# Kernel optimization log

Measured on AMD Instinct MI355X. Metric: run time of the kernel, lower is better.

The kernel has to match this reference:

```python
import jax, jax.numpy as jnp
import numpy as np

N = 50000   # nodes
E = 800000  # edges (before self loops)
F = 128     # in_dim
H = 4       # heads
C = 32      # hidden_dim per head
HC = H * C  # 128 == F
L = 3       # n_layers
G = 64      # graphs in batch
OUT = 64    # out_dim
NEG_SLOPE = 0.2


def setup_inputs() -> dict:
    key = jax.random.key(0)
    ks = jax.random.split(key, 12)
    s = 0.1
    x = jax.random.normal(ks[0], (N, F), jnp.float32)
    src = jax.random.randint(ks[1], (E,), 0, N, dtype=jnp.int32)
    dst = jax.random.randint(ks[2], (E,), 0, N, dtype=jnp.int32)
    # even split into G graphs so no graph is empty (segment_max safe)
    batch = (jnp.arange(N, dtype=jnp.int32) * G // N).astype(jnp.int32)
    Ws = jax.random.normal(ks[3], (L, HC, HC), jnp.float32) * s       # layer0 in=F=HC
    att_src = jax.random.normal(ks[4], (L, H, C), jnp.float32) * s
    att_dst = jax.random.normal(ks[5], (L, H, C), jnp.float32) * s
    conv_b = jnp.zeros((L, HC), jnp.float32)
    gate_W = jax.random.normal(ks[6], (L + 1, HC, 1), jnp.float32) * s
    gate_b = jnp.zeros((L + 1,), jnp.float32)
    lin_W = jax.random.normal(ks[7], (L + 1, HC, OUT), jnp.float32) * s
    lin_b = jnp.zeros((L + 1, OUT), jnp.float32)
    h_weights = jnp.ones((L + 1,), jnp.float32) / (L + 1)
    h0 = jax.random.normal(ks[8], (1,), jnp.float32)
    beta = jax.random.normal(ks[9], (OUT,), jnp.float32) * s
    pool_w = jnp.ones((3,), jnp.float32) / 3.0
    return dict(x=x, src=src, dst=dst, batch=batch, Ws=Ws, att_src=att_src,
                att_dst=att_dst, conv_b=conv_b, gate_W=gate_W, gate_b=gate_b,
                lin_W=lin_W, lin_b=lin_b, h_weights=h_weights, h0=h0,
                beta=beta, pool_w=pool_w)


def _seg_softmax(e, idx, n):
    # numerically stable softmax within segments
    m = jax.ops.segment_max(e, idx, num_segments=n)
    m = jnp.where(jnp.isfinite(m), m, 0.0)
    ex = jnp.exp(e - m[idx])
    s = jax.ops.segment_sum(ex, idx, num_segments=n)
    return ex / (s[idx] + 1e-16)


def _gat_layer(x, src, dst, W, a_src, a_dst, b):
    h = (x @ W).reshape(N, H, C)               # [N,H,C]
    al_s = jnp.sum(h * a_src, axis=-1)         # [N,H]
    al_d = jnp.sum(h * a_dst, axis=-1)         # [N,H]
    e = jax.nn.leaky_relu(al_s[src] + al_d[dst], NEG_SLOPE)  # [E+N,H]
    alpha = _seg_softmax(e, dst, N)            # softmax over incoming edges
    msg = h[src] * alpha[..., None]            # [E+N,H,C]
    out = jax.ops.segment_sum(msg, dst, num_segments=N)
    return out.reshape(N, HC) + b


def _pool_block(x, gw, gb, pool_w, batch, counts):
    gate = jax.nn.sigmoid(x @ gw + gb)[:, 0]          # [N]
    a = _seg_softmax(gate, batch, G)                  # per-graph attention
    p_att = jax.ops.segment_sum(a[:, None] * x, batch, num_segments=G)
    p_mean = jax.ops.segment_sum(x, batch, num_segments=G) / counts[:, None]
    p_max = jax.ops.segment_max(x, batch, num_segments=G)
    return pool_w[0] * p_att + pool_w[1] * p_mean + pool_w[2] * p_max


def reference(x, src, dst, batch, Ws, att_src, att_dst, conv_b, gate_W,
              gate_b, lin_W, lin_b, h_weights, h0, beta, pool_w):
    loops = jnp.arange(N, dtype=src.dtype)
    src_sl = jnp.concatenate([src, loops])
    dst_sl = jnp.concatenate([dst, loops])
    counts = jax.ops.segment_sum(jnp.ones((N,), x.dtype), batch, num_segments=G)
    out = jnp.zeros((G, OUT), x.dtype)
    for i in range(L):
        p = _pool_block(x, gate_W[i], gate_b[i], pool_w, batch, counts)
        out = out + h_weights[i] * (p @ lin_W[i] + lin_b[i])
        x = _gat_layer(x, src_sl, dst_sl, Ws[i], att_src[i], att_dst[i], conv_b[i])
        if i != L - 1:
            x = jax.nn.relu(x)
    p = _pool_block(x, gate_W[L], gate_b[L], pool_w, batch, counts)
    out = out + h_weights[L] * (p @ lin_W[L] + lin_b[L])
    risk_score = out @ beta + h0[0]   # [G]
    return risk_score
```

## Files before the change

kernel.cpp:

```cpp
#include <hip/hip_runtime.h>
#include <hip/hip_fp16.h>
#include <math.h>

#define N_NODES 50000
#define N_EDGES 800000
#define HC 128
#define NH 4
#define NG 64
#define NOUT 64
#define NLAYERS 3
#define POOL_CHUNKS 16
#define CAST_BLOCKS (N_NODES * HC / 4 / 256)
#define PREPW_BLOCKS (NLAYERS * HC * HC / 256)
#define NBKT ((N_NODES + 127) / 128)
#define PB_BLOCKS ((N_EDGES + 4095) / 4096)
#define GEMM_BLOCKS ((N_NODES + 15) / 16)
#define POOL2_BLOCKS (NG * POOL_CHUNKS / 2)
#define XT_STRIDE 136
#define ZREG_FLOATS ((NLAYERS + 1) * NG * HC * 2 + (NLAYERS + 1) * NG)
#define ZREG_BLOCKS ((ZREG_FLOATS / 4 + 255) / 256)
#define PMAX_BLOCKS ((NLAYERS + 1) * NG * HC / 4 / 256)
#define LOG2E 1.44269504f

typedef _Float16 v4h __attribute__((ext_vector_type(4)));
typedef float v4f __attribute__((ext_vector_type(4)));

__device__ __forceinline__ void graph_range(int g, int* start, int* end) {
    *start = (int)(((long long)g * N_NODES + NG - 1) / NG);
    *end   = (int)(((long long)(g + 1) * N_NODES + NG - 1) / NG);
}

__device__ __forceinline__ float atomicMaxFloat(float* addr, float val) {
    if (val >= 0.f)
        return __int_as_float(atomicMax((int*)addr, __float_as_int(val)));
    else
        return __uint_as_float(atomicMin((unsigned int*)addr, __float_as_uint(val)));
}


__device__ __forceinline__ void gemm_body(
        int b, const __half* __restrict__ x, const _Float16* __restrict__ Wt,
        const float* __restrict__ a_src, const float* __restrict__ a_dst,
        __half* __restrict__ hh, float* __restrict__ al_s, float* __restrict__ al_d) {
    __shared__ __align__(16) _Float16 xt[16][XT_STRIDE];
    int t = threadIdx.x;
    int w = t >> 6;
    int l = t & 63;
    int n0 = b * 16;
    {
        uint4 v = ((const uint4*)(x + (size_t)n0 * HC))[t];
        *(uint4*)&xt[t >> 4][(t & 15) * 8] = v;
    }
    __syncthreads();
    int m = l & 15;
    int kg = (l >> 4) * 4;
    v4h a[8];
#pragma unroll
    for (int ks = 0; ks < 8; ks++)
        a[ks] = *(const v4h*)&xt[m][kg + ks * 16];
    __syncthreads();
    const _Float16* bp0 = Wt + (uint)(w * 32 + m) * HC + kg;
    const _Float16* bp1 = bp0 + 16 * HC;
    v4f acc0 = {0.f, 0.f, 0.f, 0.f}, acc1 = {0.f, 0.f, 0.f, 0.f};
#pragma unroll
    for (int ks = 0; ks < 8; ks++) {
        v4h b0 = *(const v4h*)(bp0 + ks * 16);
        v4h b1 = *(const v4h*)(bp1 + ks * 16);
        acc0 = __builtin_amdgcn_mfma_f32_16x16x16f16(a[ks], b0, acc0, 0, 0, 0);
        acc1 = __builtin_amdgcn_mfma_f32_16x16x16f16(a[ks], b1, acc1, 0, 0, 0);
    }
    int d0 = w * 32 + m;
    float as0 = a_src[d0] * LOG2E,      ad0 = a_dst[d0] * LOG2E;
    float as1 = a_src[d0 + 16] * LOG2E, ad1 = a_dst[d0 + 16] * LOG2E;
    int rloc = (l >> 4) * 4;
#pragma unroll
    for (int r = 0; r < 4; r++) {
        int n = n0 + rloc + r;
        xt[rloc + r][d0]      = (_Float16)acc0[r];
        xt[rloc + r][d0 + 16] = (_Float16)acc1[r];
        float vs = acc0[r] * as0 + acc1[r] * as1;
        float vd = acc0[r] * ad0 + acc1[r] * ad1;
#pragma unroll
        for (int mk = 8; mk >= 1; mk >>= 1) {
            vs += __shfl_xor(vs, mk);
            vd += __shfl_xor(vd, mk);
        }
        if ((l & 15) == 0) {
            al_s[(uint)(n * NH + w)] = vs;
            al_d[(uint)(n * NH + w)] = vd;
        }
    }
    __syncthreads();
    uint4 v = *(const uint4*)&xt[t >> 4][(t & 15) * 8];
    ((uint4*)(hh + (size_t)n0 * HC))[t] = v;
}

__device__ __forceinline__ void pool_body(
        int b, const __half* __restrict__ x, const float* __restrict__ gate,
        float* __restrict__ p_att, float* __restrict__ p_sum,
        float* __restrict__ p_max, float* __restrict__ wsum) {
    int c = b * 2 + (threadIdx.x >> 7);
    int g = c >> 4;
    int chunk = c & 15;
    int d = threadIdx.x & 127;
    int start, end; graph_range(g, &start, &end);
    int cnt = end - start;
    int cstart = start + (cnt * chunk) / POOL_CHUNKS;
    int cend   = start + (cnt * (chunk + 1)) / POOL_CHUNKS;
    float aat = 0.f, asu = 0.f, amx = -INFINITY, ws = 0.f;
    int n = cstart;
    for (; n + 4 <= cend; n += 4) {
        float w0 = gate[n],     w1 = gate[n + 1];
        float w2 = gate[n + 2], w3 = gate[n + 3];
        float x0 = __half2float(x[(uint)((n + 0) * HC + d)]);
        float x1 = __half2float(x[(uint)((n + 1) * HC + d)]);
        float x2 = __half2float(x[(uint)((n + 2) * HC + d)]);
        float x3 = __half2float(x[(uint)((n + 3) * HC + d)]);
        aat = fmaf(w0, x0, aat); aat = fmaf(w1, x1, aat);
        aat = fmaf(w2, x2, aat); aat = fmaf(w3, x3, aat);
        asu += (x0 + x1) + (x2 + x3);
        amx = fmaxf(amx, fmaxf(fmaxf(x0, x1), fmaxf(x2, x3)));
        ws += (w0 + w1) + (w2 + w3);
    }
    for (; n < cend; n++) {
        float w = gate[n];
        float xv = __half2float(x[(uint)(n * HC + d)]);
        aat = fmaf(w, xv, aat);
        asu += xv;
        amx = fmaxf(amx, xv);
        ws += w;
    }
    atomicAdd(&p_att[g * HC + d], aat);
    atomicAdd(&p_sum[g * HC + d], asu);
    atomicMaxFloat(&p_max[g * HC + d], amx);
    if (d == 0) atomicAdd(&wsum[g], ws);
}

__device__ __forceinline__ void scat2_body(
        int bkt, const int2* __restrict__ part, const int* __restrict__ bktbase,
        int* __restrict__ rowptr, int* __restrict__ csr_src) {
    __shared__ int degs[128];
    __shared__ int curs[128];
    __shared__ int w0tot;
    int t = threadIdx.x;
    int nstart = bkt << 7;
    int nend = nstart + 128; if (nend > N_NODES) nend = N_NODES;
    int nloc = nend - nstart;
    int estart = bktbase[bkt], eend = bktbase[bkt + 1];
    if (t < 128) degs[t] = 0;
    __syncthreads();
    for (int e = estart + t; e < eend; e += 256)
        atomicAdd(&degs[part[e].y - nstart], 1);
    __syncthreads();
    int v = 0, inc = 0;
    if (t < 128) {
        v = degs[t];
        inc = v;
#pragma unroll
        for (int off = 1; off < 64; off <<= 1) {
            int u = __shfl_up(inc, off);
            if ((t & 63) >= off) inc += u;
        }
    }
    if (t == 63) w0tot = inc;
    __syncthreads();
    if (t < 128) {
        int excl = inc - v + ((t >= 64) ? w0tot : 0);
        int rp = estart + excl;
        curs[t] = rp;
        if (t < nloc) rowptr[nstart + t] = rp;
    }
    __syncthreads();
    for (int e = estart + t; e < eend; e += 256) {
        int2 p = part[e];
        int pos = atomicAdd(&curs[p.y - nstart], 1);
        csr_src[pos] = p.x;
    }
}


__global__ __launch_bounds__(256) void k_prep(
        const float* __restrict__ x, __half* __restrict__ xh,
        const float* __restrict__ Ws, _Float16* __restrict__ Wt,
        const int* __restrict__ dst, int* __restrict__ bh,
        const float* __restrict__ gw, const float* __restrict__ gbp,
        float* __restrict__ gate,
        float* __restrict__ zreg, uint* __restrict__ pmaxw) {
    int b = blockIdx.x;
    int t = threadIdx.x;
    if (b < CAST_BLOCKS) {
        uint i = b * 256 + t;
        float4 v = ((const float4*)x)[i];
        __half2 a = __floats2half2_rn(v.x, v.y);
        __half2 c = __floats2half2_rn(v.z, v.w);
        ((__half2*)xh)[2 * i] = a;
        ((__half2*)xh)[2 * i + 1] = c;
        float4 gwv = ((const float4*)gw)[t & 31];
        float dot = v.x * gwv.x + v.y * gwv.y + v.z * gwv.z + v.w * gwv.w;
#pragma unroll
        for (int m = 16; m >= 1; m >>= 1) dot += __shfl_xor(dot, m);
        if ((t & 31) == 0) {
            int n = b * 8 + (t >> 5);
            float sg = 1.f / (1.f + __expf(-(dot + gbp[0])));
            gate[n] = __expf(sg);
        }
    } else if (b < CAST_BLOCKS + PREPW_BLOCKS) {
        int e = (b - CAST_BLOCKS) * 256 + t;
        int layer = e >> 14; int r = e & 16383; int k = r >> 7; int d = r & 127;
        Wt[layer * 16384 + d * 128 + k] = (_Float16)Ws[layer * 16384 + k * 128 + d];
    } else if (b < CAST_BLOCKS + PREPW_BLOCKS + PB_BLOCKS) {
        int pb = b - CAST_BLOCKS - PREPW_BLOCKS;
        __shared__ int cnt[NBKT];
        for (int i = t; i < NBKT; i += 256) cnt[i] = 0;
        __syncthreads();
        int base = pb * 4096;
#pragma unroll
        for (int k = 0; k < 16; k++) {
            int e = base + t + 256 * k;
            if (e < N_EDGES) atomicAdd(&cnt[dst[e] >> 7], 1);
        }
        __syncthreads();
        for (int i = t; i < NBKT; i += 256) bh[i * PB_BLOCKS + pb] = cnt[i];
    } else {
        int zb = b - CAST_BLOCKS - PREPW_BLOCKS - PB_BLOCKS;
        if (zb < ZREG_BLOCKS) {
            int i = zb * 256 + t;
            if (i < ZREG_FLOATS / 4)
                ((float4*)zreg)[i] = make_float4(0.f, 0.f, 0.f, 0.f);
        } else {
            int i = (zb - ZREG_BLOCKS) * 256 + t;
            uint4 f; f.x = f.y = f.z = f.w = 0xFFFFFFFFu;
            ((uint4*)pmaxw)[i] = f;
        }
    }
}

__global__ __launch_bounds__(256) void k_scan_bh(int* __restrict__ bh,
                                                 int* __restrict__ bkttot) {
    __shared__ int tmp[256];
    int bkt = blockIdx.x, t = threadIdx.x;
    int v = (t < PB_BLOCKS) ? bh[bkt * PB_BLOCKS + t] : 0;
    tmp[t] = v;
    __syncthreads();
    for (int off = 1; off < 256; off <<= 1) {
        int u = (t >= off) ? tmp[t - off] : 0;
        __syncthreads();
        tmp[t] += u;
        __syncthreads();
    }
    if (t < PB_BLOCKS) bh[bkt * PB_BLOCKS + t] = tmp[t] - v;
    if (t == 255) bkttot[bkt] = tmp[255];
}

__global__ __launch_bounds__(512) void k_bktbase(const int* __restrict__ bkttot,
                                                 int* __restrict__ bktbase,
                                                 int* __restrict__ rowptr) {
    __shared__ int tmp[512];
    int t = threadIdx.x;
    int v = (t < NBKT) ? bkttot[t] : 0;
    tmp[t] = v;
    __syncthreads();
    for (int off = 1; off < 512; off <<= 1) {
        int u = (t >= off) ? tmp[t - off] : 0;
        __syncthreads();
        tmp[t] += u;
        __syncthreads();
    }
    if (t < NBKT) bktbase[t] = tmp[t] - v;
    if (t == NBKT - 1) {
        bktbase[NBKT] = tmp[t];
        rowptr[N_NODES] = tmp[t];
    }
}

__global__ __launch_bounds__(256) void k_part(
        const int* __restrict__ src, const int* __restrict__ dst,
        const int* __restrict__ bktbase, const int* __restrict__ bh,
        int2* __restrict__ part) {
    __shared__ int curs[NBKT];
    int blk = blockIdx.x, t = threadIdx.x;
    for (int i = t; i < NBKT; i += 256)
        curs[i] = bktbase[i] + bh[i * PB_BLOCKS + blk];
    __syncthreads();
    int base = blk * 4096;
#pragma unroll
    for (int k = 0; k < 16; k++) {
        int e = base + t + 256 * k;
        if (e < N_EDGES) {
            int d = dst[e];
            int pos = atomicAdd(&curs[d >> 7], 1);
            part[pos] = make_int2(src[e], d);
        }
    }
}


__global__ __launch_bounds__(256) void k_fused_a2(
        const int2* __restrict__ part, const int* __restrict__ bktbase,
        int* __restrict__ rowptr, int* __restrict__ csr_src,
        const __half* __restrict__ x0h, const _Float16* __restrict__ Wt,
        const float* __restrict__ a_src, const float* __restrict__ a_dst,
        __half* __restrict__ hh, float* __restrict__ al_s, float* __restrict__ al_d,
        const float* __restrict__ gate,
        float* __restrict__ p_att, float* __restrict__ p_sum,
        float* __restrict__ p_max, float* __restrict__ wsum) {
    int b = blockIdx.x;
    if (b < NBKT) {
        scat2_body(b, part, bktbase, rowptr, csr_src);
    } else if (b < NBKT + GEMM_BLOCKS) {
        gemm_body(b - NBKT, x0h, Wt, a_src, a_dst, hh, al_s, al_d);
    } else {
        pool_body(b - NBKT - GEMM_BLOCKS, x0h, gate, p_att, p_sum, p_max, wsum);
    }
}

__global__ __launch_bounds__(256) void k_fused_b(
        const __half* __restrict__ x, const _Float16* __restrict__ Wt,
        const float* __restrict__ a_src, const float* __restrict__ a_dst,
        __half* __restrict__ hh, float* __restrict__ al_s, float* __restrict__ al_d,
        const float* __restrict__ gate,
        float* __restrict__ p_att, float* __restrict__ p_sum,
        float* __restrict__ p_max, float* __restrict__ wsum) {
    int b = blockIdx.x;
    if (b < GEMM_BLOCKS) {
        gemm_body(b, x, Wt, a_src, a_dst, hh, al_s, al_d);
    } else {
        pool_body(b - GEMM_BLOCKS, x, gate, p_att, p_sum, p_max, wsum);
    }
}

__global__ __launch_bounds__(256) void k_pool(
        const __half* __restrict__ x, const float* __restrict__ gate,
        float* __restrict__ p_att, float* __restrict__ p_sum,
        float* __restrict__ p_max, float* __restrict__ wsum) {
    pool_body(blockIdx.x, x, gate, p_att, p_sum, p_max, wsum);
}


__global__ __launch_bounds__(256) void k_agg(
        const __half* __restrict__ hh, const float* __restrict__ al_s,
        const float* __restrict__ al_d, const int* __restrict__ rowptr,
        const int* __restrict__ csr_src, const float* __restrict__ conv_b,
        __half* __restrict__ xout, int do_relu,
        const float* __restrict__ gw, const float* __restrict__ gbp,
        float* __restrict__ gate) {
    int n = (blockIdx.x * blockDim.x + threadIdx.x) >> 6;
    if (n >= N_NODES) return;
    int l = threadIdx.x & 63;
    int head = l >> 4;
    int le = l & 15;
    int grp4 = (l & 48) << 2;
    float ad = al_d[(uint)(n * NH + head)];
    const __half2* hh2 = (const __half2*)hh;
    float e0 = al_s[(uint)(n * NH + head)] + ad;
    e0 = fmaxf(e0, 0.2f * e0);
    float s_uni = exp2f(e0);
    float2 vself = __half22float2(hh2[(uint)(n * 64 + l)]);
    float ax = s_uni * vself.x, ay = s_uni * vself.y;
    int jb = rowptr[n], je = rowptr[n + 1];
    float s_part = 0.f;
    for (int j = jb; j < je; j += 16) {
        int rem = je - j;
        bool act = le < rem;
        int my_s = csr_src[j + (act ? le : 0)];
        float aa = al_s[(uint)(my_s * NH + head)];
        float e = aa + ad;
        e = fmaxf(e, 0.2f * e);
        float ex = act ? exp2f(e) : 0.f;
        s_part += ex;
        int exb = __float_as_int(ex);
        __half2 vv[16];
#pragma unroll
        for (int u = 0; u < 16; u++) {
            int ssu = __builtin_amdgcn_readlane(my_s, u);
            const __half2* rp = hh2 + ((size_t)(uint)ssu << 6);
            vv[u] = rp[l];
        }
#pragma unroll
        for (int u = 0; u < 16; u++) {
            float exu = __int_as_float(
                __builtin_amdgcn_ds_bpermute(grp4 + 4 * u, exb));
            float2 vf = __half22float2(vv[u]);
            ax = fmaf(exu, vf.x, ax);
            ay = fmaf(exu, vf.y, ay);
        }
    }
    s_part += __shfl_xor(s_part, 1);
    s_part += __shfl_xor(s_part, 2);
    s_part += __shfl_xor(s_part, 4);
    s_part += __shfl_xor(s_part, 8);
    float s = s_part + s_uni;
    float inv = 1.f / (s + 1e-16f);
    float2 cb = ((const float2*)conv_b)[l];
    float r0 = fmaf(ax, inv, cb.x);
    float r1 = fmaf(ay, inv, cb.y);
    if (do_relu) { r0 = fmaxf(r0, 0.f); r1 = fmaxf(r1, 0.f); }
    ((__half2*)xout)[(uint)(n * 64 + l)] = __floats2half2_rn(r0, r1);
    float2 gwv = ((const float2*)gw)[l];
    float gv = r0 * gwv.x + r1 * gwv.y;
#pragma unroll
    for (int m = 32; m >= 1; m >>= 1) gv += __shfl_xor(gv, m);
    if (l == 0) {
        float sg = 1.f / (1.f + __expf(-(gv + gbp[0])));
        gate[n] = __expf(sg);
    }
}


__global__ __launch_bounds__(128) void k_finish(
        const float* __restrict__ p_att, const float* __restrict__ p_sum,
        const float* __restrict__ p_max, const float* __restrict__ wsum,
        const float* __restrict__ pool_w, const float* __restrict__ lin_W,
        const float* __restrict__ lin_b, const float* __restrict__ hw,
        const float* __restrict__ beta, const float* __restrict__ h0,
        float* __restrict__ out) {
    int g = blockIdx.x, t = threadIdx.x;
    __shared__ float p[NLAYERS + 1][HC];
    int start, end; graph_range(g, &start, &end);
    float cinv = 1.f / (float)(end - start);
    float pw0 = pool_w[0], pw1 = pool_w[1], pw2 = pool_w[2];
#pragma unroll
    for (int j = 0; j <= NLAYERS; j++) {
        float winv = 1.f / (wsum[j * NG + g] + 1e-16f);
        p[j][t] = pw0 * p_att[(j * NG + g) * HC + t] * winv
                + pw1 * p_sum[(j * NG + g) * HC + t] * cinv
                + pw2 * p_max[(j * NG + g) * HC + t];
    }
    __syncthreads();
    if (t < NOUT) {
        float acc = 0.f;
#pragma unroll
        for (int j = 0; j <= NLAYERS; j++) {
            float a = lin_b[j * NOUT + t];
            const float* Wj = lin_W + (size_t)j * HC * NOUT;
            for (int k = 0; k < HC; k++) a = fmaf(p[j][k], Wj[k * NOUT + t], a);
            acc = fmaf(hw[j], a, acc);
        }
        float v = acc * beta[t];
#pragma unroll
        for (int m = 32; m >= 1; m >>= 1) v += __shfl_xor(v, m);
        if (t == 0) out[g] = v + h0[0];
    }
}


extern "C" void kernel_launch(void* const* d_in, const int* in_sizes, int n_in,
                              void* d_out, int out_size, void* d_ws, size_t ws_size,
                              hipStream_t stream) {
    const float* x0       = (const float*)d_in[0];
    const int*   src      = (const int*)d_in[1];
    const int*   dst      = (const int*)d_in[2];
    const float* Ws       = (const float*)d_in[4];
    const float* att_src  = (const float*)d_in[5];
    const float* att_dst  = (const float*)d_in[6];
    const float* conv_b   = (const float*)d_in[7];
    const float* gate_W   = (const float*)d_in[8];
    const float* gate_b   = (const float*)d_in[9];
    const float* lin_W    = (const float*)d_in[10];
    const float* lin_b    = (const float*)d_in[11];
    const float* h_w      = (const float*)d_in[12];
    const float* h0       = (const float*)d_in[13];
    const float* beta     = (const float*)d_in[14];
    const float* pool_w   = (const float*)d_in[15];

    char* base = (char*)d_ws;
    size_t off = 0;
    auto carve = [&](size_t bytes) -> char* {
        char* p = base + off;
        off = (off + bytes + 255) & ~(size_t)255;
        return p;
    };
    __half*    x0h     = (__half*)carve((size_t)N_NODES * HC * 2);
    __half*    xA      = (__half*)carve((size_t)N_NODES * HC * 2);
    __half*    xB      = (__half*)carve((size_t)N_NODES * HC * 2);
    __half*    hh      = (__half*)carve((size_t)N_NODES * HC * 2);
    _Float16*  Wt      = (_Float16*)carve((size_t)NLAYERS * HC * HC * 2);
    float*     al_s    = (float*)carve((size_t)N_NODES * NH * 4);
    float*     al_d    = (float*)carve((size_t)N_NODES * NH * 4);
    float*     gate    = (float*)carve((size_t)N_NODES * 4);
    int*       rowptr  = (int*)carve((size_t)(N_NODES + 1) * 4);
    int*       csrsrc  = (int*)carve((size_t)N_EDGES * 4);
    int*       bh      = (int*)carve((size_t)NBKT * PB_BLOCKS * 4);
    int*       bkttot  = (int*)carve((size_t)NBKT * 4);
    int*       bktbase = (int*)carve((size_t)(NBKT + 1) * 4);
    int2*      part    = (int2*)carve((size_t)N_EDGES * 8);
    float*     zreg    = (float*)carve((size_t)ZREG_FLOATS * 4);
    float*     p_att   = zreg;
    float*     p_sum   = zreg + (size_t)(NLAYERS + 1) * NG * HC;
    float*     wsum    = p_sum + (size_t)(NLAYERS + 1) * NG * HC;
    float*     p_max   = (float*)carve((size_t)(NLAYERS + 1) * NG * HC * 4);

    k_prep<<<CAST_BLOCKS + PREPW_BLOCKS + PB_BLOCKS + ZREG_BLOCKS + PMAX_BLOCKS,
             256, 0, stream>>>(
        x0, x0h, Ws, Wt, dst, bh, gate_W, gate_b, gate, zreg, (uint*)p_max);

    k_scan_bh<<<NBKT, 256, 0, stream>>>(bh, bkttot);
    k_bktbase<<<1, 512, 0, stream>>>(bkttot, bktbase, rowptr);
    k_part<<<PB_BLOCKS, 256, 0, stream>>>(src, dst, bktbase, bh, part);

    k_fused_a2<<<NBKT + GEMM_BLOCKS + POOL2_BLOCKS, 256, 0, stream>>>(
        part, bktbase, rowptr, csrsrc,
        x0h, Wt, att_src, att_dst, hh, al_s, al_d,
        gate, p_att, p_sum, p_max, wsum);

    __half* xbufs[3] = { xA, xB, xA };
    for (int i = 0; i < NLAYERS; i++) {
        __half* xnext = xbufs[i];
        int j = i + 1;
        k_agg<<<(N_NODES + 3) / 4, 256, 0, stream>>>(hh, al_s, al_d, rowptr, csrsrc,
                                                     conv_b + i * HC, xnext,
                                                     (i != NLAYERS - 1) ? 1 : 0,
                                                     gate_W + j * HC, gate_b + j,
                                                     gate);
        if (i + 1 < NLAYERS) {
            k_fused_b<<<GEMM_BLOCKS + POOL2_BLOCKS, 256, 0, stream>>>(
                xnext, Wt + (size_t)(i + 1) * HC * HC,
                att_src + (i + 1) * HC, att_dst + (i + 1) * HC,
                hh, al_s, al_d,
                gate,
                p_att + (size_t)j * NG * HC,
                p_sum + (size_t)j * NG * HC,
                p_max + (size_t)j * NG * HC,
                wsum + j * NG);
        } else {
            k_pool<<<POOL2_BLOCKS, 256, 0, stream>>>(
                xnext, gate,
                p_att + (size_t)j * NG * HC,
                p_sum + (size_t)j * NG * HC,
                p_max + (size_t)j * NG * HC,
                wsum + j * NG);
        }
    }

    k_finish<<<NG, 128, 0, stream>>>(p_att, p_sum, p_max, wsum, pool_w,
                                     lin_W, lin_b, h_w, beta, h0, (float*)d_out);
}
```

Baseline: 270.9 us.

## Fuse input cast and gate into first GEMM, pack edge partitions, reschedule pooling

The fp32→fp16 cast of x and the gate computation move out of the prep kernel and into the first GEMM, which reads fp32 x directly and writes x0h. Edge partition entries are packed into one int (16-bit src, 7-bit local dst), which halves partition traffic but relies on N fitting in 16 bits. Layer-0 pooling now runs in the same launch as the first aggregation, with double-buffered gate arrays, so more independent work shares each launch. The bpermute broadcast in aggregation is replaced by ds_swizzle.

Result: faster. 264.5 us (-2.4%).

```diff
diff --git a/kernel.cpp b/kernel.cpp
--- a/kernel.cpp
+++ b/kernel.cpp
@@ -10,12 +10,12 @@
 #define NOUT 64
 #define NLAYERS 3
 #define POOL_CHUNKS 16
-#define CAST_BLOCKS (N_NODES * HC / 4 / 256)
 #define PREPW_BLOCKS (NLAYERS * HC * HC / 256)
 #define NBKT ((N_NODES + 127) / 128)
 #define PB_BLOCKS ((N_EDGES + 4095) / 4096)
 #define GEMM_BLOCKS ((N_NODES + 15) / 16)
 #define POOL2_BLOCKS (NG * POOL_CHUNKS / 2)
+#define AGG_BLOCKS ((N_NODES + 3) / 4)
 #define XT_STRIDE 136
 #define ZREG_FLOATS ((NLAYERS + 1) * NG * HC * 2 + (NLAYERS + 1) * NG)
 #define ZREG_BLOCKS ((ZREG_FLOATS / 4 + 255) / 256)
@@ -38,17 +38,51 @@
 }
 
 
+template<bool F32>
 __device__ __forceinline__ void gemm_body(
-        int b, const __half* __restrict__ x, const _Float16* __restrict__ Wt,
+        int b, const void* xin, const _Float16* __restrict__ Wt,
         const float* __restrict__ a_src, const float* __restrict__ a_dst,
-        __half* __restrict__ hh, float* __restrict__ al_s, float* __restrict__ al_d) {
+        __half* __restrict__ hh, float* __restrict__ al_s, float* __restrict__ al_d,
+        __half* __restrict__ xh_out, const float* __restrict__ gw,
+        const float* __restrict__ gbp, float* __restrict__ gate) {
     __shared__ __align__(16) _Float16 xt[16][XT_STRIDE];
     int t = threadIdx.x;
     int w = t >> 6;
     int l = t & 63;
     int n0 = b * 16;
-    {
-        uint4 v = ((const uint4*)(x + (size_t)n0 * HC))[t];
+    if constexpr (F32) {
+        const float4* xg = (const float4*)((const float*)xin + (size_t)n0 * HC);
+        float4 v0 = xg[t];
+        float4 v1 = xg[t + 256];
+        float4 gwv = ((const float4*)gw)[t & 31];
+        float p0 = v0.x * gwv.x + v0.y * gwv.y + v0.z * gwv.z + v0.w * gwv.w;
+        float p1 = v1.x * gwv.x + v1.y * gwv.y + v1.z * gwv.z + v1.w * gwv.w;
+#pragma unroll
+        for (int mk = 16; mk >= 1; mk >>= 1) {
+            p0 += __shfl_xor(p0, mk);
+            p1 += __shfl_xor(p1, mk);
+        }
+        if ((t & 31) == 0) {
+            int r = t >> 5;
+            float sg0 = 1.f / (1.f + __expf(-(p0 + gbp[0])));
+            float sg1 = 1.f / (1.f + __expf(-(p1 + gbp[0])));
+            gate[n0 + r]     = __expf(sg0);
+            gate[n0 + 8 + r] = __expf(sg1);
+        }
+        __half2 h00 = __floats2half2_rn(v0.x, v0.y);
+        __half2 h01 = __floats2half2_rn(v0.z, v0.w);
+        __half2 h10 = __floats2half2_rn(v1.x, v1.y);
+        __half2 h11 = __floats2half2_rn(v1.z, v1.w);
+        uint2 pa, pb;
+        pa.x = *(const uint*)&h00; pa.y = *(const uint*)&h01;
+        pb.x = *(const uint*)&h10; pb.y = *(const uint*)&h11;
+        int row = t >> 5, colh = (t & 31) * 4;
+        *(uint2*)&xt[row][colh] = pa;
+        *(uint2*)&xt[row + 8][colh] = pb;
+        ((uint2*)xh_out)[(size_t)n0 * (HC / 4) + t]       = pa;
+        ((uint2*)xh_out)[(size_t)n0 * (HC / 4) + t + 256] = pb;
+    } else {
+        uint4 v = ((const uint4*)((const __half*)xin + (size_t)n0 * HC))[t];
         *(uint4*)&xt[t >> 4][(t & 15) * 8] = v;
     }
     __syncthreads();
@@ -137,7 +171,7 @@
 }
 
 __device__ __forceinline__ void scat2_body(
-        int bkt, const int2* __restrict__ part, const int* __restrict__ bktbase,
+        int bkt, const int* __restrict__ part, const int* __restrict__ bktbase,
         int* __restrict__ rowptr, int* __restrict__ csr_src) {
     __shared__ int degs[128];
     __shared__ int curs[128];
@@ -150,7 +184,7 @@
     if (t < 128) degs[t] = 0;
     __syncthreads();
     for (int e = estart + t; e < eend; e += 256)
-        atomicAdd(&degs[part[e].y - nstart], 1);
+        atomicAdd(&degs[(part[e] >> 16) & 127], 1);
     __syncthreads();
     int v = 0, inc = 0;
     if (t < 128) {
@@ -172,184 +206,24 @@
     }
     __syncthreads();
     for (int e = estart + t; e < eend; e += 256) {
-        int2 p = part[e];
-        int pos = atomicAdd(&curs[p.y - nstart], 1);
-        csr_src[pos] = p.x;
-    }
-}
-
-
-__global__ __launch_bounds__(256) void k_prep(
-        const float* __restrict__ x, __half* __restrict__ xh,
-        const float* __restrict__ Ws, _Float16* __restrict__ Wt,
-        const int* __restrict__ dst, int* __restrict__ bh,
-        const float* __restrict__ gw, const float* __restrict__ gbp,
-        float* __restrict__ gate,
-        float* __restrict__ zreg, uint* __restrict__ pmaxw) {
-    int b = blockIdx.x;
-    int t = threadIdx.x;
-    if (b < CAST_BLOCKS) {
-        uint i = b * 256 + t;
-        float4 v = ((const float4*)x)[i];
-        __half2 a = __floats2half2_rn(v.x, v.y);
-        __half2 c = __floats2half2_rn(v.z, v.w);
-        ((__half2*)xh)[2 * i] = a;
-        ((__half2*)xh)[2 * i + 1] = c;
-        float4 gwv = ((const float4*)gw)[t & 31];
-        float dot = v.x * gwv.x + v.y * gwv.y + v.z * gwv.z + v.w * gwv.w;
-#pragma unroll
-        for (int m = 16; m >= 1; m >>= 1) dot += __shfl_xor(dot, m);
-        if ((t & 31) == 0) {
-            int n = b * 8 + (t >> 5);
-            float sg = 1.f / (1.f + __expf(-(dot + gbp[0])));
-            gate[n] = __expf(sg);
-        }
-    } else if (b < CAST_BLOCKS + PREPW_BLOCKS) {
-        int e = (b - CAST_BLOCKS) * 256 + t;
-        int layer = e >> 14; int r = e & 16383; int k = r >> 7; int d = r & 127;
-        Wt[layer * 16384 + d * 128 + k] = (_Float16)Ws[layer * 16384 + k * 128 + d];
-    } else if (b < CAST_BLOCKS + PREPW_BLOCKS + PB_BLOCKS) {
-        int pb = b - CAST_BLOCKS - PREPW_BLOCKS;
-        __shared__ int cnt[NBKT];
-        for (int i = t; i < NBKT; i += 256) cnt[i] = 0;
-        __syncthreads();
-        int base = pb * 4096;
-#pragma unroll
-        for (int k = 0; k < 16; k++) {
-            int e = base + t + 256 * k;
-            if (e < N_EDGES) atomicAdd(&cnt[dst[e] >> 7], 1);
-        }
-        __syncthreads();
-        for (int i = t; i < NBKT; i += 256) bh[i * PB_BLOCKS + pb] = cnt[i];
-    } else {
-        int zb = b - CAST_BLOCKS - PREPW_BLOCKS - PB_BLOCKS;
-        if (zb < ZREG_BLOCKS) {
-            int i = zb * 256 + t;
-            if (i < ZREG_FLOATS / 4)
-                ((float4*)zreg)[i] = make_float4(0.f, 0.f, 0.f, 0.f);
-        } else {
-            int i = (zb - ZREG_BLOCKS) * 256 + t;
-            uint4 f; f.x = f.y = f.z = f.w = 0xFFFFFFFFu;
-            ((uint4*)pmaxw)[i] = f;
-        }
-    }
-}
-
-__global__ __launch_bounds__(256) void k_scan_bh(int* __restrict__ bh,
-                                                 int* __restrict__ bkttot) {
-    __shared__ int tmp[256];
-    int bkt = blockIdx.x, t = threadIdx.x;
-    int v = (t < PB_BLOCKS) ? bh[bkt * PB_BLOCKS + t] : 0;
-    tmp[t] = v;
-    __syncthreads();
-    for (int off = 1; off < 256; off <<= 1) {
-        int u = (t >= off) ? tmp[t - off] : 0;
-        __syncthreads();
-        tmp[t] += u;
-        __syncthreads();
-    }
-    if (t < PB_BLOCKS) bh[bkt * PB_BLOCKS + t] = tmp[t] - v;
-    if (t == 255) bkttot[bkt] = tmp[255];
-}
-
-__global__ __launch_bounds__(512) void k_bktbase(const int* __restrict__ bkttot,
-                                                 int* __restrict__ bktbase,
-                                                 int* __restrict__ rowptr) {
-    __shared__ int tmp[512];
-    int t = threadIdx.x;
-    int v = (t < NBKT) ? bkttot[t] : 0;
-    tmp[t] = v;
-    __syncthreads();
-    for (int off = 1; off < 512; off <<= 1) {
-        int u = (t >= off) ? tmp[t - off] : 0;
-        __syncthreads();
-        tmp[t] += u;
-        __syncthreads();
-    }
-    if (t < NBKT) bktbase[t] = tmp[t] - v;
-    if (t == NBKT - 1) {
-        bktbase[NBKT] = tmp[t];
-        rowptr[N_NODES] = tmp[t];
-    }
-}
-
-__global__ __launch_bounds__(256) void k_part(
-        const int* __restrict__ src, const int* __restrict__ dst,
-        const int* __restrict__ bktbase, const int* __restrict__ bh,
-        int2* __restrict__ part) {
-    __shared__ int curs[NBKT];
-    int blk = blockIdx.x, t = threadIdx.x;
-    for (int i = t; i < NBKT; i += 256)
-        curs[i] = bktbase[i] + bh[i * PB_BLOCKS + blk];
-    __syncthreads();
-    int base = blk * 4096;
-#pragma unroll
-    for (int k = 0; k < 16; k++) {
-        int e = base + t + 256 * k;
-        if (e < N_EDGES) {
-            int d = dst[e];
-            int pos = atomicAdd(&curs[d >> 7], 1);
-            part[pos] = make_int2(src[e], d);
-        }
-    }
-}
-
-
-__global__ __launch_bounds__(256) void k_fused_a2(
-        const int2* __restrict__ part, const int* __restrict__ bktbase,
-        int* __restrict__ rowptr, int* __restrict__ csr_src,
-        const __half* __restrict__ x0h, const _Float16* __restrict__ Wt,
-        const float* __restrict__ a_src, const float* __restrict__ a_dst,
-        __half* __restrict__ hh, float* __restrict__ al_s, float* __restrict__ al_d,
-        const float* __restrict__ gate,
-        float* __restrict__ p_att, float* __restrict__ p_sum,
-        float* __restrict__ p_max, float* __restrict__ wsum) {
-    int b = blockIdx.x;
-    if (b < NBKT) {
-        scat2_body(b, part, bktbase, rowptr, csr_src);
-    } else if (b < NBKT + GEMM_BLOCKS) {
-        gemm_body(b - NBKT, x0h, Wt, a_src, a_dst, hh, al_s, al_d);
-    } else {
-        pool_body(b - NBKT - GEMM_BLOCKS, x0h, gate, p_att, p_sum, p_max, wsum);
-    }
-}
-
-__global__ __launch_bounds__(256) void k_fused_b(
-        const __half* __restrict__ x, const _Float16* __restrict__ Wt,
-        const float* __restrict__ a_src, const float* __restrict__ a_dst,
-        __half* __restrict__ hh, float* __restrict__ al_s, float* __restrict__ al_d,
-        const float* __restrict__ gate,
-        float* __restrict__ p_att, float* __restrict__ p_sum,
-        float* __restrict__ p_max, float* __restrict__ wsum) {
-    int b = blockIdx.x;
-    if (b < GEMM_BLOCKS) {
-        gemm_body(b, x, Wt, a_src, a_dst, hh, al_s, al_d);
-    } else {
-        pool_body(b - GEMM_BLOCKS, x, gate, p_att, p_sum, p_max, wsum);
-    }
-}
-
-__global__ __launch_bounds__(256) void k_pool(
-        const __half* __restrict__ x, const float* __restrict__ gate,
-        float* __restrict__ p_att, float* __restrict__ p_sum,
-        float* __restrict__ p_max, float* __restrict__ wsum) {
-    pool_body(blockIdx.x, x, gate, p_att, p_sum, p_max, wsum);
-}
-
-
-__global__ __launch_bounds__(256) void k_agg(
-        const __half* __restrict__ hh, const float* __restrict__ al_s,
+        int p = part[e];
+        int pos = atomicAdd(&curs[(p >> 16) & 127], 1);
+        csr_src[pos] = p & 0xFFFF;
+    }
+}
+
+__device__ __forceinline__ void agg_body(
+        int b, const __half* __restrict__ hh, const float* __restrict__ al_s,
         const float* __restrict__ al_d, const int* __restrict__ rowptr,
         const int* __restrict__ csr_src, const float* __restrict__ conv_b,
         __half* __restrict__ xout, int do_relu,
         const float* __restrict__ gw, const float* __restrict__ gbp,
         float* __restrict__ gate) {
-    int n = (blockIdx.x * blockDim.x + threadIdx.x) >> 6;
+    int n = b * 4 + (threadIdx.x >> 6);
     if (n >= N_NODES) return;
     int l = threadIdx.x & 63;
     int head = l >> 4;
     int le = l & 15;
-    int grp4 = (l & 48) << 2;
     float ad = al_d[(uint)(n * NH + head)];
     const __half2* hh2 = (const __half2*)hh;
     float e0 = al_s[(uint)(n * NH + head)] + ad;
@@ -376,14 +250,18 @@
             const __half2* rp = hh2 + ((size_t)(uint)ssu << 6);
             vv[u] = rp[l];
         }
-#pragma unroll
-        for (int u = 0; u < 16; u++) {
-            float exu = __int_as_float(
-                __builtin_amdgcn_ds_bpermute(grp4 + 4 * u, exb));
-            float2 vf = __half22float2(vv[u]);
-            ax = fmaf(exu, vf.x, ax);
-            ay = fmaf(exu, vf.y, ay);
-        }
+#define AGG_SLOT(U) {                                                        \
+            float exu = __int_as_float(                                      \
+                __builtin_amdgcn_ds_swizzle(exb, 16 + 32 * (U)));            \
+            float2 vf = __half22float2(vv[U]);                               \
+            ax = fmaf(exu, vf.x, ax);                                        \
+            ay = fmaf(exu, vf.y, ay);                                        \
+        }
+        AGG_SLOT(0)  AGG_SLOT(1)  AGG_SLOT(2)  AGG_SLOT(3)
+        AGG_SLOT(4)  AGG_SLOT(5)  AGG_SLOT(6)  AGG_SLOT(7)
+        AGG_SLOT(8)  AGG_SLOT(9)  AGG_SLOT(10) AGG_SLOT(11)
+        AGG_SLOT(12) AGG_SLOT(13) AGG_SLOT(14) AGG_SLOT(15)
+#undef AGG_SLOT
     }
     s_part += __shfl_xor(s_part, 1);
     s_part += __shfl_xor(s_part, 2);
@@ -404,6 +282,174 @@
         float sg = 1.f / (1.f + __expf(-(gv + gbp[0])));
         gate[n] = __expf(sg);
     }
+}
+
+
+__global__ __launch_bounds__(256) void k_prep(
+        const float* __restrict__ Ws, _Float16* __restrict__ Wt,
+        const int* __restrict__ dst, int* __restrict__ bh,
+        float* __restrict__ zreg, uint* __restrict__ pmaxw) {
+    int b = blockIdx.x;
+    int t = threadIdx.x;
+    if (b < PREPW_BLOCKS) {
+        int e = b * 256 + t;
+        int layer = e >> 14; int r = e & 16383; int k = r >> 7; int d = r & 127;
+        Wt[layer * 16384 + d * 128 + k] = (_Float16)Ws[layer * 16384 + k * 128 + d];
+    } else if (b < PREPW_BLOCKS + PB_BLOCKS) {
+        int pb = b - PREPW_BLOCKS;
+        __shared__ int cnt[NBKT];
+        for (int i = t; i < NBKT; i += 256) cnt[i] = 0;
+        __syncthreads();
+        int base = pb * 4096;
+#pragma unroll
+        for (int k = 0; k < 16; k++) {
+            int e = base + t + 256 * k;
+            if (e < N_EDGES) atomicAdd(&cnt[dst[e] >> 7], 1);
+        }
+        __syncthreads();
+        for (int i = t; i < NBKT; i += 256) bh[i * PB_BLOCKS + pb] = cnt[i];
+    } else {
+        int zb = b - PREPW_BLOCKS - PB_BLOCKS;
+        if (zb < ZREG_BLOCKS) {
+            int i = zb * 256 + t;
+            if (i < ZREG_FLOATS / 4)
+                ((float4*)zreg)[i] = make_float4(0.f, 0.f, 0.f, 0.f);
+        } else {
+            int i = (zb - ZREG_BLOCKS) * 256 + t;
+            uint4 f; f.x = f.y = f.z = f.w = 0xFFFFFFFFu;
+            ((uint4*)pmaxw)[i] = f;
+        }
+    }
+}
+
+__global__ __launch_bounds__(256) void k_scan_bh(int* __restrict__ bh,
+                                                 int* __restrict__ bkttot) {
+    __shared__ int tmp[256];
+    int bkt = blockIdx.x, t = threadIdx.x;
+    int v = (t < PB_BLOCKS) ? bh[bkt * PB_BLOCKS + t] : 0;
+    tmp[t] = v;
+    __syncthreads();
+    for (int off = 1; off < 256; off <<= 1) {
+        int u = (t >= off) ? tmp[t - off] : 0;
+        __syncthreads();
+        tmp[t] += u;
+        __syncthreads();
+    }
+    if (t < PB_BLOCKS) bh[bkt * PB_BLOCKS + t] = tmp[t] - v;
+    if (t == 255) bkttot[bkt] = tmp[255];
+}
+
+__global__ __launch_bounds__(512) void k_bktbase(const int* __restrict__ bkttot,
+                                                 int* __restrict__ bktbase,
+                                                 int* __restrict__ rowptr) {
+    __shared__ int tmp[512];
+    int t = threadIdx.x;
+    int v = (t < NBKT) ? bkttot[t] : 0;
+    tmp[t] = v;
+    __syncthreads();
+    for (int off = 1; off < 512; off <<= 1) {
+        int u = (t >= off) ? tmp[t - off] : 0;
+        __syncthreads();
+        tmp[t] += u;
+        __syncthreads();
+    }
+    if (t < NBKT) bktbase[t] = tmp[t] - v;
+    if (t == NBKT - 1) {
+        bktbase[NBKT] = tmp[t];
+        rowptr[N_NODES] = tmp[t];
+    }
+}
+
+__global__ __launch_bounds__(256) void k_part(
+        const int* __restrict__ src, const int* __restrict__ dst,
+        const int* __restrict__ bktbase, const int* __restrict__ bh,
+        int* __restrict__ part) {
+    __shared__ int curs[NBKT];
+    int blk = blockIdx.x, t = threadIdx.x;
+    for (int i = t; i < NBKT; i += 256)
+        curs[i] = bktbase[i] + bh[i * PB_BLOCKS + blk];
+    __syncthreads();
+    int base = blk * 4096;
+#pragma unroll
+    for (int k = 0; k < 16; k++) {
+        int e = base + t + 256 * k;
+        if (e < N_EDGES) {
+            int d = dst[e];
+            int pos = atomicAdd(&curs[d >> 7], 1);
+            part[pos] = src[e] | ((d & 127) << 16);
+        }
+    }
+}
+
+
+__global__ __launch_bounds__(256) void k_fused_a2(
+        const int* __restrict__ part, const int* __restrict__ bktbase,
+        int* __restrict__ rowptr, int* __restrict__ csr_src,
+        const float* __restrict__ x0, const _Float16* __restrict__ Wt,
+        const float* __restrict__ a_src, const float* __restrict__ a_dst,
+        __half* __restrict__ hh, float* __restrict__ al_s, float* __restrict__ al_d,
+        __half* __restrict__ x0h, const float* __restrict__ gw,
+        const float* __restrict__ gbp, float* __restrict__ gate) {
+    int b = blockIdx.x;
+    if (b < NBKT) {
+        scat2_body(b, part, bktbase, rowptr, csr_src);
+    } else {
+        gemm_body<true>(b - NBKT, x0, Wt, a_src, a_dst, hh, al_s, al_d,
+                        x0h, gw, gbp, gate);
+    }
+}
+
+__global__ __launch_bounds__(256) void k_fused_agg(
+        const __half* __restrict__ hh, const float* __restrict__ al_s,
+        const float* __restrict__ al_d, const int* __restrict__ rowptr,
+        const int* __restrict__ csr_src, const float* __restrict__ conv_b,
+        __half* __restrict__ xout, int do_relu,
+        const float* __restrict__ gw, const float* __restrict__ gbp,
+        float* __restrict__ gate_out,
+        const __half* __restrict__ xp, const float* __restrict__ gate_in,
+        float* __restrict__ p_att, float* __restrict__ p_sum,
+        float* __restrict__ p_max, float* __restrict__ wsum) {
+    int b = blockIdx.x;
+    if (b < POOL2_BLOCKS) {
+        pool_body(b, xp, gate_in, p_att, p_sum, p_max, wsum);
+    } else {
+        agg_body(b - POOL2_BLOCKS, hh, al_s, al_d, rowptr, csr_src, conv_b,
+                 xout, do_relu, gw, gbp, gate_out);
+    }
+}
+
+__global__ __launch_bounds__(256) void k_fused_b(
+        const __half* __restrict__ x, const _Float16* __restrict__ Wt,
+        const float* __restrict__ a_src, const float* __restrict__ a_dst,
+        __half* __restrict__ hh, float* __restrict__ al_s, float* __restrict__ al_d,
+        const float* __restrict__ gate,
+        float* __restrict__ p_att, float* __restrict__ p_sum,
+        float* __restrict__ p_max, float* __restrict__ wsum) {
+    int b = blockIdx.x;
+    if (b < GEMM_BLOCKS) {
+        gemm_body<false>(b, x, Wt, a_src, a_dst, hh, al_s, al_d,
+                         nullptr, nullptr, nullptr, nullptr);
+    } else {
+        pool_body(b - GEMM_BLOCKS, x, gate, p_att, p_sum, p_max, wsum);
+    }
+}
+
+__global__ __launch_bounds__(256) void k_agg(
+        const __half* __restrict__ hh, const float* __restrict__ al_s,
+        const float* __restrict__ al_d, const int* __restrict__ rowptr,
+        const int* __restrict__ csr_src, const float* __restrict__ conv_b,
+        __half* __restrict__ xout, int do_relu,
+        const float* __restrict__ gw, const float* __restrict__ gbp,
+        float* __restrict__ gate) {
+    agg_body(blockIdx.x, hh, al_s, al_d, rowptr, csr_src, conv_b,
+             xout, do_relu, gw, gbp, gate);
+}
+
+__global__ __launch_bounds__(256) void k_pool(
+        const __half* __restrict__ x, const float* __restrict__ gate,
+        float* __restrict__ p_att, float* __restrict__ p_sum,
+        float* __restrict__ p_max, float* __restrict__ wsum) {
+    pool_body(blockIdx.x, x, gate, p_att, p_sum, p_max, wsum);
 }
 
 
@@ -477,60 +523,61 @@
     _Float16*  Wt      = (_Float16*)carve((size_t)NLAYERS * HC * HC * 2);
     float*     al_s    = (float*)carve((size_t)N_NODES * NH * 4);
     float*     al_d    = (float*)carve((size_t)N_NODES * NH * 4);
-    float*     gate    = (float*)carve((size_t)N_NODES * 4);
+    float*     gateA   = (float*)carve((size_t)N_NODES * 4);
+    float*     gateB   = (float*)carve((size_t)N_NODES * 4);
     int*       rowptr  = (int*)carve((size_t)(N_NODES + 1) * 4);
     int*       csrsrc  = (int*)carve((size_t)N_EDGES * 4);
     int*       bh      = (int*)carve((size_t)NBKT * PB_BLOCKS * 4);
     int*       bkttot  = (int*)carve((size_t)NBKT * 4);
     int*       bktbase = (int*)carve((size_t)(NBKT + 1) * 4);
-    int2*      part    = (int2*)carve((size_t)N_EDGES * 8);
+    int*       part    = (int*)carve((size_t)N_EDGES * 4);
     float*     zreg    = (float*)carve((size_t)ZREG_FLOATS * 4);
     float*     p_att   = zreg;
     float*     p_sum   = zreg + (size_t)(NLAYERS + 1) * NG * HC;
     float*     wsum    = p_sum + (size_t)(NLAYERS + 1) * NG * HC;
     float*     p_max   = (float*)carve((size_t)(NLAYERS + 1) * NG * HC * 4);
 
-    k_prep<<<CAST_BLOCKS + PREPW_BLOCKS + PB_BLOCKS + ZREG_BLOCKS + PMAX_BLOCKS,
-             256, 0, stream>>>(
-        x0, x0h, Ws, Wt, dst, bh, gate_W, gate_b, gate, zreg, (uint*)p_max);
+    k_prep<<<PREPW_BLOCKS + PB_BLOCKS + ZREG_BLOCKS + PMAX_BLOCKS, 256, 0, stream>>>(
+        Ws, Wt, dst, bh, zreg, (uint*)p_max);
 
     k_scan_bh<<<NBKT, 256, 0, stream>>>(bh, bkttot);
     k_bktbase<<<1, 512, 0, stream>>>(bkttot, bktbase, rowptr);
     k_part<<<PB_BLOCKS, 256, 0, stream>>>(src, dst, bktbase, bh, part);
 
-    k_fused_a2<<<NBKT + GEMM_BLOCKS + POOL2_BLOCKS, 256, 0, stream>>>(
+    k_fused_a2<<<NBKT + GEMM_BLOCKS, 256, 0, stream>>>(
         part, bktbase, rowptr, csrsrc,
-        x0h, Wt, att_src, att_dst, hh, al_s, al_d,
-        gate, p_att, p_sum, p_max, wsum);
-
-    __half* xbufs[3] = { xA, xB, xA };
-    for (int i = 0; i < NLAYERS; i++) {
-        __half* xnext = xbufs[i];
-        int j = i + 1;
-        k_agg<<<(N_NODES + 3) / 4, 256, 0, stream>>>(hh, al_s, al_d, rowptr, csrsrc,
-                                                     conv_b + i * HC, xnext,
-                                                     (i != NLAYERS - 1) ? 1 : 0,
-                                                     gate_W + j * HC, gate_b + j,
-                                                     gate);
-        if (i + 1 < NLAYERS) {
-            k_fused_b<<<GEMM_BLOCKS + POOL2_BLOCKS, 256, 0, stream>>>(
-                xnext, Wt + (size_t)(i + 1) * HC * HC,
-                att_src + (i + 1) * HC, att_dst + (i + 1) * HC,
-                hh, al_s, al_d,
-                gate,
-                p_att + (size_t)j * NG * HC,
-                p_sum + (size_t)j * NG * HC,
-                p_max + (size_t)j * NG * HC,
-                wsum + j * NG);
-        } else {
-            k_pool<<<POOL2_BLOCKS, 256, 0, stream>>>(
-                xnext, gate,
-                p_att + (size_t)j * NG * HC,
-                p_sum + (size_t)j * NG * HC,
-                p_max + (size_t)j * NG * HC,
-                wsum + j * NG);
-        }
-    }
+        x0, Wt, att_src, att_dst, hh, al_s, al_d,
+        x0h, gate_W, gate_b, gateA);
+
+    k_fused_agg<<<POOL2_BLOCKS + AGG_BLOCKS, 256, 0, stream>>>(
+        hh, al_s, al_d, rowptr, csrsrc, conv_b,
+        xA, 1, gate_W + HC, gate_b + 1, gateB,
+        x0h, gateA, p_att, p_sum, p_max, wsum);
+
+    k_fused_b<<<GEMM_BLOCKS + POOL2_BLOCKS, 256, 0, stream>>>(
+        xA, Wt + (size_t)1 * HC * HC, att_src + HC, att_dst + HC,
+        hh, al_s, al_d, gateB,
+        p_att + (size_t)1 * NG * HC, p_sum + (size_t)1 * NG * HC,
+        p_max + (size_t)1 * NG * HC, wsum + 1 * NG);
+
+    k_agg<<<AGG_BLOCKS, 256, 0, stream>>>(
+        hh, al_s, al_d, rowptr, csrsrc, conv_b + HC,
+        xB, 1, gate_W + 2 * HC, gate_b + 2, gateA);
+
+    k_fused_b<<<GEMM_BLOCKS + POOL2_BLOCKS, 256, 0, stream>>>(
+        xB, Wt + (size_t)2 * HC * HC, att_src + 2 * HC, att_dst + 2 * HC,
+        hh, al_s, al_d, gateA,
+        p_att + (size_t)2 * NG * HC, p_sum + (size_t)2 * NG * HC,
+        p_max + (size_t)2 * NG * HC, wsum + 2 * NG);
+
+    k_agg<<<AGG_BLOCKS, 256, 0, stream>>>(
+        hh, al_s, al_d, rowptr, csrsrc, conv_b + 2 * HC,
+        xA, 0, gate_W + 3 * HC, gate_b + 3, gateB);
+
+    k_pool<<<POOL2_BLOCKS, 256, 0, stream>>>(
+        xA, gateB,
+        p_att + (size_t)3 * NG * HC, p_sum + (size_t)3 * NG * HC,
+        p_max + (size_t)3 * NG * HC, wsum + 3 * NG);
 
     k_finish<<<NG, 128, 0, stream>>>(p_att, p_sum, p_max, wsum, pool_w,
                                      lin_W, lin_b, h_w, beta, h0, (float*)d_out);
```
